# Kernel tuning notes

Measured on AMD Instinct MI355X. Metric: run time of the kernel, lower is better.

## Reference

```python
import jax, jax.numpy as jnp
import numpy as np

RES = 0.025
X_MIN, Z_MIN, Z_MAX = -1.6, 0.1, 3.3
D = 128
MIN_DEPTH = Z_MIN + RES / 2.0                      # 0.1125
MAX_DEPTH = MIN_DEPTH + RES * D - RES              # 3.2875
BEV_H, BEV_W = 128, 128
CAM_OFFSET = np.array([X_MIN, 0.0, -Z_MAX], dtype=np.float32)
LOG_UNIFORM3 = -1.0986  # torch code's constant fill = log(1/3)
EPS = 1e-07


def setup_inputs() -> dict:
    key = jax.random.key(0)
    k1, k2 = jax.random.split(key)
    B, H, W = 2, 256, 256
    depth_logits = jax.random.normal(k1, (B, D, H, W), dtype=jnp.float32)
    bev_logits = jax.random.normal(k2, (B, 2, BEV_H, BEV_W), dtype=jnp.float32)
    # realistic inverse intrinsics: focal 85.333 at 128px, scaled to W
    f = 85.333 * (W / 128.0)
    K = np.eye(4, dtype=np.float32)
    K[0, 0] = f; K[1, 1] = f; K[0, 2] = W / 2.0; K[1, 2] = H / 2.0
    inv_K = jnp.asarray(np.tile(np.linalg.inv(K)[None], (B, 1, 1)))
    return {"depth_logits": depth_logits, "bev_logits": bev_logits, "inv_K": inv_K}


def reference(depth_logits, bev_logits, inv_K):
    B, _, H, W = depth_logits.shape
    N = H * W

    # depth distribution
    depth_logprobs = jax.nn.log_softmax(depth_logits, axis=1)          # [B,D,H,W]
    dvals = jnp.linspace(MIN_DEPTH, MAX_DEPTH, D).astype(jnp.float32)  # [D]

    # pixel homogeneous coords (meshgrid indexing='xy': row0 = x, row1 = y)
    xg = jnp.tile(jnp.arange(W, dtype=jnp.float32)[None, :], (H, 1)).reshape(-1)
    yg = jnp.tile(jnp.arange(H, dtype=jnp.float32)[:, None], (1, W)).reshape(-1)
    pix = jnp.stack([xg, yg, jnp.ones_like(xg)], axis=0)               # [3,N]

    cam = jnp.einsum('bij,jn->bin', inv_K[:, :3, :3], pix)             # [B,3,N]
    # lift along depth bins -> [B,N,D,3]
    pts = dvals[None, :, None, None] * cam[:, None, :, :]              # [B,D,3,N]
    pts = pts.transpose(0, 3, 1, 2).reshape(-1, 3)                     # [B*N*D,3]
    pts = pts * jnp.array([1.0, -1.0, -1.0], dtype=jnp.float32)
    # torch .long() truncates toward zero, matched by astype(int32)
    vox = ((pts - jnp.asarray(CAM_OFFSET)) / RES).astype(jnp.int32)    # [B*N*D,3]
    bix = jnp.repeat(jnp.arange(B, dtype=jnp.int32), N * D)            # [B*N*D]

    valid = ((vox[:, 0] >= 0) & (vox[:, 0] < BEV_W)
             & (vox[:, 2] >= 0) & (vox[:, 2] < BEV_H)
             & (vox[:, 1] <= 0))

    # BEV 3-class probabilities
    p = jnp.clip(jax.nn.sigmoid(bev_logits), EPS, 1.0 - EPS)           # [B,2,128,128]
    p0, p1 = p[:, 0], p[:, 1]
    class_probs = jnp.stack([1.0 - p1, p1 * p0, p1 * (1.0 - p0)], axis=1)  # [B,3,Hb,Wb]
    cp_flat = class_probs.reshape(-1)

    base = vox[:, 0] + BEV_W * vox[:, 2] + BEV_W * BEV_H * 3 * bix     # [B*N*D]
    safe_base = jnp.where(valid, base, 0)
    cell = BEV_W * BEV_H
    lifted = []
    for C in range(3):
        probs = jnp.take(cp_flat, safe_base + cell * C)
        lifted.append(jnp.where(valid, jnp.log(probs), LOG_UNIFORM3))
    B_lifted = jnp.stack(lifted, axis=-1).reshape(B, N, D, 3)

    dlp = depth_logprobs.reshape(B, D, N).transpose(0, 2, 1)           # [B,N,D]
    combined = (B_lifted + dlp[..., None]).reshape(B, H, W, D, 3)
    return combined
```

## Files before the change

### kernel.cpp

```cpp
#include <hip/hip_runtime.h>
#include <math.h>

#define DD    128
#define HH    256
#define WW    256
#define BEVN  16384
#define LOG3  (-1.0986f)

__global__ void jd_logcp_kernel(const float* __restrict__ bev,
                                float* __restrict__ logcp, int B) {
    int i = blockIdx.x * blockDim.x + threadIdx.x;
    if (i >= B * BEVN) return;
    int b  = i >> 14;
    int zx = i & (BEVN - 1);
    float x0 = bev[(b * 2 + 0) * BEVN + zx];
    float x1 = bev[(b * 2 + 1) * BEVN + zx];
    const float LO = 1e-7f;
    const float HI = (float)(1.0 - 1e-7);
    float p0 = fminf(fmaxf(1.0f / (1.0f + expf(-x0)), LO), HI);
    float p1 = fminf(fmaxf(1.0f / (1.0f + expf(-x1)), LO), HI);
    float c0 = 1.0f - p1;
    float c1 = p1 * p0;
    float c2 = p1 * (1.0f - p0);
    float* o = logcp + (size_t)b * (3 * BEVN) + zx;
    o[0]         = logf(c0);
    o[BEVN]      = logf(c1);
    o[2 * BEVN]  = logf(c2);
}

__global__ __launch_bounds__(256) void jd_main_kernel(
        const float* __restrict__ depth, const float* __restrict__ invK,
        const float* __restrict__ logcp, float* __restrict__ out) {
    __shared__ float tile[DD * 65];
    __shared__ float pmax[4 * 64];
    __shared__ float psum[4 * 64];

    const int t    = threadIdx.x;
    const int lane = t & 63;
    const int q    = t >> 6;
    const int bid  = blockIdx.x;
    const int w0   = (bid & 3) * 64;
    const int h    = (bid >> 2) & (HH - 1);
    const int b    = bid >> 10;

    const float* dp = depth + ((size_t)b * DD) * (HH * WW) + (size_t)h * WW + w0 + lane;
    const int dbase = q * 32;
    float v[32];
    float m = -INFINITY;
#pragma unroll
    for (int i = 0; i < 32; ++i) {
        v[i] = dp[(size_t)(dbase + i) * (HH * WW)];
        m = fmaxf(m, v[i]);
    }
    pmax[q * 64 + lane] = m;
    __syncthreads();
    float mm = fmaxf(fmaxf(pmax[lane], pmax[64 + lane]),
                     fmaxf(pmax[128 + lane], pmax[192 + lane]));
    float s = 0.0f;
#pragma unroll
    for (int i = 0; i < 32; ++i) s += expf(v[i] - mm);
    psum[q * 64 + lane] = s;
    __syncthreads();
    float S  = ((psum[lane] + psum[64 + lane]) + psum[128 + lane]) + psum[192 + lane];
    float lS = logf(S);
#pragma unroll
    for (int i = 0; i < 32; ++i)
        tile[(dbase + i) * 65 + lane] = (v[i] - mm) - lS;
    __syncthreads();

    const float* ik = invK + b * 16;
    const float ik00 = ik[0], ik01 = ik[1], ik02 = ik[2];
    const float ik10 = ik[4], ik11 = ik[5], ik12 = ik[6];
    const float ik20 = ik[8], ik21 = ik[9], ik22 = ik[10];

    const double stepd = (3.2875 - 0.1125) / 127.0;
    const int dA = lane, dB = lane + 64;
    const float dvA = (dA == 127) ? (float)3.2875 : (float)((double)dA * stepd + 0.1125);
    const float dvB = (dB == 127) ? (float)3.2875 : (float)((double)dB * stepd + 0.1125);

    const float* cp = logcp + (size_t)b * (3 * BEVN);
    const size_t pixbase0 = ((size_t)b * (HH * WW) + (size_t)h * WW + w0) * (DD * 3);
    const float yf = (float)h;

    for (int wi = 0; wi < 16; ++wi) {
        const int w = wi * 4 + q;
        const float xf = (float)(w0 + w);
        const float camx = __fadd_rn(__fadd_rn(__fmul_rn(ik00, xf), __fmul_rn(ik01, yf)), ik02);
        const float camy = __fadd_rn(__fadd_rn(__fmul_rn(ik10, xf), __fmul_rn(ik11, yf)), ik12);
        const float camz = __fadd_rn(__fadd_rn(__fmul_rn(ik20, xf), __fmul_rn(ik21, yf)), ik22);
        float* op = out + pixbase0 + (size_t)w * (DD * 3);
#pragma unroll
        for (int half = 0; half < 2; ++half) {
            const int d = half * 64 + lane;
            const float dval = half ? dvB : dvA;
            const float dlp = tile[d * 65 + w];
            float px = __fmul_rn(dval, camx);
            float py = __fmul_rn(dval, camy);
            float pz = __fmul_rn(dval, camz);
            py = -py; pz = -pz;
            const float tx = __fsub_rn(px, -1.6f);
            const float ty = __fsub_rn(py, 0.0f);
            const float tz = __fsub_rn(pz, -3.3f);
            const int vx = (int)__fdiv_rn(tx, 0.025f);
            const int vy = (int)__fdiv_rn(ty, 0.025f);
            const int vz = (int)__fdiv_rn(tz, 0.025f);
            const bool valid = (vx >= 0) & (vx < 128) & (vz >= 0) & (vz < 128) & (vy <= 0);
            const int base = valid ? (vz * 128 + vx) : 0;
            const float l0 = cp[base];
            const float l1 = cp[base + BEVN];
            const float l2 = cp[base + 2 * BEVN];
            const float e0 = __fadd_rn(valid ? l0 : LOG3, dlp);
            const float e1 = __fadd_rn(valid ? l1 : LOG3, dlp);
            const float e2 = __fadd_rn(valid ? l2 : LOG3, dlp);
            op[d * 3 + 0] = e0;
            op[d * 3 + 1] = e1;
            op[d * 3 + 2] = e2;
        }
    }
}

extern "C" void kernel_launch(void* const* d_in, const int* in_sizes, int n_in,
                              void* d_out, int out_size, void* d_ws, size_t ws_size,
                              hipStream_t stream) {
    const float* depth = (const float*)d_in[0];
    const float* bev   = (const float*)d_in[1];
    const float* invK  = (const float*)d_in[2];
    float* out = (float*)d_out;
    float* logcp = (float*)d_ws;

    const int B = in_sizes[0] / (DD * HH * WW);

    jd_logcp_kernel<<<(B * BEVN + 255) / 256, 256, 0, stream>>>(bev, logcp, B);
    jd_main_kernel<<<B * HH * (WW / 64), 256, 0, stream>>>(depth, invK, logcp, out);
}
```

Baseline: 315.9 us.

## Remap threads to pixels, interleave BEV log-probs, stage vectorized stores via LDS

```diff
diff --git a/kernel.cpp b/kernel.cpp
--- a/kernel.cpp
+++ b/kernel.cpp
@@ -1,11 +1,12 @@
 #include <hip/hip_runtime.h>
 #include <math.h>
 
-#define DD    128
-#define HH    256
-#define WW    256
-#define BEVN  16384
-#define LOG3  (-1.0986f)
+#define DD   128
+#define HH   256
+#define WW   256
+#define HW   (HH * WW)
+#define BEVN 16384
+#define LOG3 (-1.0986f)
 
 __global__ void jd_logcp_kernel(const float* __restrict__ bev,
                                 float* __restrict__ logcp, int B) {
@@ -19,21 +20,18 @@
     const float HI = (float)(1.0 - 1e-7);
     float p0 = fminf(fmaxf(1.0f / (1.0f + expf(-x0)), LO), HI);
     float p1 = fminf(fmaxf(1.0f / (1.0f + expf(-x1)), LO), HI);
-    float c0 = 1.0f - p1;
-    float c1 = p1 * p0;
-    float c2 = p1 * (1.0f - p0);
-    float* o = logcp + (size_t)b * (3 * BEVN) + zx;
-    o[0]         = logf(c0);
-    o[BEVN]      = logf(c1);
-    o[2 * BEVN]  = logf(c2);
+    float* o = logcp + ((size_t)b * BEVN + zx) * 3;
+    o[0] = logf(1.0f - p1);
+    o[1] = logf(p1 * p0);
+    o[2] = logf(p1 * (1.0f - p0));
 }
 
 __global__ __launch_bounds__(256) void jd_main_kernel(
         const float* __restrict__ depth, const float* __restrict__ invK,
         const float* __restrict__ logcp, float* __restrict__ out) {
-    __shared__ float tile[DD * 65];
-    __shared__ float pmax[4 * 64];
-    __shared__ float psum[4 * 64];
+    __shared__ float stg[4 * 13 * 64];
+    __shared__ float pmax[256];
+    __shared__ float psum[256];
 
     const int t    = threadIdx.x;
     const int lane = t & 63;
@@ -42,58 +40,61 @@
     const int w0   = (bid & 3) * 64;
     const int h    = (bid >> 2) & (HH - 1);
     const int b    = bid >> 10;
+    const int dbase = q * 32;
 
-    const float* dp = depth + ((size_t)b * DD) * (HH * WW) + (size_t)h * WW + w0 + lane;
-    const int dbase = q * 32;
+    const float* dp = depth + (size_t)b * DD * HW + (size_t)h * WW + w0 + lane;
     float v[32];
     float m = -INFINITY;
 #pragma unroll
     for (int i = 0; i < 32; ++i) {
-        v[i] = dp[(size_t)(dbase + i) * (HH * WW)];
+        v[i] = dp[(size_t)(dbase + i) * HW];
         m = fmaxf(m, v[i]);
     }
-    pmax[q * 64 + lane] = m;
+    pmax[t] = m;
     __syncthreads();
     float mm = fmaxf(fmaxf(pmax[lane], pmax[64 + lane]),
                      fmaxf(pmax[128 + lane], pmax[192 + lane]));
     float s = 0.0f;
 #pragma unroll
     for (int i = 0; i < 32; ++i) s += expf(v[i] - mm);
-    psum[q * 64 + lane] = s;
+    psum[t] = s;
     __syncthreads();
     float S  = ((psum[lane] + psum[64 + lane]) + psum[128 + lane]) + psum[192 + lane];
     float lS = logf(S);
 #pragma unroll
-    for (int i = 0; i < 32; ++i)
-        tile[(dbase + i) * 65 + lane] = (v[i] - mm) - lS;
-    __syncthreads();
+    for (int i = 0; i < 32; ++i) v[i] = (v[i] - mm) - lS;
 
     const float* ik = invK + b * 16;
-    const float ik00 = ik[0], ik01 = ik[1], ik02 = ik[2];
-    const float ik10 = ik[4], ik11 = ik[5], ik12 = ik[6];
-    const float ik20 = ik[8], ik21 = ik[9], ik22 = ik[10];
+    const float yf = (float)h;
+    const float xf = (float)(w0 + lane);
+    const float camx = __fadd_rn(__fadd_rn(__fmul_rn(ik[0], xf), __fmul_rn(ik[1], yf)), ik[2]);
+    const float camy = __fadd_rn(__fadd_rn(__fmul_rn(ik[4], xf), __fmul_rn(ik[5], yf)), ik[6]);
+    const float camz = __fadd_rn(__fadd_rn(__fmul_rn(ik[8], xf), __fmul_rn(ik[9], yf)), ik[10]);
+
+    const float* cp3 = logcp + (size_t)b * BEVN * 3;
+    float* wstg = stg + q * (13 * 64);
+    const size_t pixbase0 = ((size_t)b * HW + (size_t)h * WW + w0) * (DD * 3);
+
+    int   ldsa[3];
+    size_t ga[3];
+#pragma unroll
+    for (int k = 0; k < 3; ++k) {
+        int g  = k * 64 + lane;
+        int ww = g / 3;
+        int kk = g - ww * 3;
+        ldsa[k] = ww * 13 + kk * 4;
+        ga[k]   = pixbase0 + (size_t)ww * (DD * 3) + (size_t)dbase * 3 + kk * 4;
+    }
 
     const double stepd = (3.2875 - 0.1125) / 127.0;
-    const int dA = lane, dB = lane + 64;
-    const float dvA = (dA == 127) ? (float)3.2875 : (float)((double)dA * stepd + 0.1125);
-    const float dvB = (dB == 127) ? (float)3.2875 : (float)((double)dB * stepd + 0.1125);
 
-    const float* cp = logcp + (size_t)b * (3 * BEVN);
-    const size_t pixbase0 = ((size_t)b * (HH * WW) + (size_t)h * WW + w0) * (DD * 3);
-    const float yf = (float)h;
-
-    for (int wi = 0; wi < 16; ++wi) {
-        const int w = wi * 4 + q;
-        const float xf = (float)(w0 + w);
-        const float camx = __fadd_rn(__fadd_rn(__fmul_rn(ik00, xf), __fmul_rn(ik01, yf)), ik02);
-        const float camy = __fadd_rn(__fadd_rn(__fmul_rn(ik10, xf), __fmul_rn(ik11, yf)), ik12);
-        const float camz = __fadd_rn(__fadd_rn(__fmul_rn(ik20, xf), __fmul_rn(ik21, yf)), ik22);
-        float* op = out + pixbase0 + (size_t)w * (DD * 3);
+    for (int sc = 0; sc < 8; ++sc) {
 #pragma unroll
-        for (int half = 0; half < 2; ++half) {
-            const int d = half * 64 + lane;
-            const float dval = half ? dvB : dvA;
-            const float dlp = tile[d * 65 + w];
+        for (int j = 0; j < 4; ++j) {
+            const int i = sc * 4 + j;
+            const int d = dbase + i;
+            const float dval = (d == 127) ? (float)3.2875
+                                          : (float)((double)d * stepd + 0.1125);
             float px = __fmul_rn(dval, camx);
             float py = __fmul_rn(dval, camy);
             float pz = __fmul_rn(dval, camz);
@@ -106,16 +107,24 @@
             const int vz = (int)__fdiv_rn(tz, 0.025f);
             const bool valid = (vx >= 0) & (vx < 128) & (vz >= 0) & (vz < 128) & (vy <= 0);
             const int base = valid ? (vz * 128 + vx) : 0;
-            const float l0 = cp[base];
-            const float l1 = cp[base + BEVN];
-            const float l2 = cp[base + 2 * BEVN];
-            const float e0 = __fadd_rn(valid ? l0 : LOG3, dlp);
-            const float e1 = __fadd_rn(valid ? l1 : LOG3, dlp);
-            const float e2 = __fadd_rn(valid ? l2 : LOG3, dlp);
-            op[d * 3 + 0] = e0;
-            op[d * 3 + 1] = e1;
-            op[d * 3 + 2] = e2;
+            const float* l = cp3 + base * 3;
+            const float l0 = l[0], l1 = l[1], l2 = l[2];
+            const float dlp = v[i];
+            wstg[lane * 13 + j * 3 + 0] = __fadd_rn(valid ? l0 : LOG3, dlp);
+            wstg[lane * 13 + j * 3 + 1] = __fadd_rn(valid ? l1 : LOG3, dlp);
+            wstg[lane * 13 + j * 3 + 2] = __fadd_rn(valid ? l2 : LOG3, dlp);
         }
+        __builtin_amdgcn_fence(__ATOMIC_ACQ_REL, "workgroup");
+#pragma unroll
+        for (int k = 0; k < 3; ++k) {
+            float4 val;
+            val.x = wstg[ldsa[k] + 0];
+            val.y = wstg[ldsa[k] + 1];
+            val.z = wstg[ldsa[k] + 2];
+            val.w = wstg[ldsa[k] + 3];
+            *(float4*)(out + ga[k] + sc * 12) = val;
+        }
+        __builtin_amdgcn_fence(__ATOMIC_ACQ_REL, "workgroup");
     }
 }
 
@@ -125,10 +134,10 @@
     const float* depth = (const float*)d_in[0];
     const float* bev   = (const float*)d_in[1];
     const float* invK  = (const float*)d_in[2];
-    float* out = (float*)d_out;
+    float* out   = (float*)d_out;
     float* logcp = (float*)d_ws;
 
-    const int B = in_sizes[0] / (DD * HH * WW);
+    const int B = in_sizes[0] / (DD * HW);
 
     jd_logcp_kernel<<<(B * BEVN + 255) / 256, 256, 0, stream>>>(bev, logcp, B);
     jd_main_kernel<<<B * HH * (WW / 64), 256, 0, stream>>>(depth, invK, logcp, out);
```

After: 396.7 us. 1.26x slower.
